# Performance work log

Hardware: AMD Instinct MI355X
Metric: run time of the kernel (lower is better)

Reference implementation:

```python
import jax, jax.numpy as jnp
import numpy as np

B, S, D, A, O = 4, 4096, 256, 64, 256

def setup_inputs() -> dict:
    key = jax.random.key(0)
    k1, k2, k3, k4, k5 = jax.random.split(key, 5)
    x = jax.random.normal(k1, (B, S, D), dtype=jnp.float32)
    # weights stored as [in, out] so projection is x @ W (same math as torch Linear W^T)
    Wk = jax.random.normal(k2, (D, A), dtype=jnp.float32) * (1.0 / np.sqrt(D))
    Wq = jax.random.normal(k3, (D, A), dtype=jnp.float32) * (1.0 / np.sqrt(D))
    Wv = jax.random.normal(k4, (D, A), dtype=jnp.float32) * (1.0 / np.sqrt(D))
    Wo = jax.random.normal(k5, (A, O), dtype=jnp.float32) * (1.0 / np.sqrt(A))
    return {"x": x, "Wk": Wk, "Wq": Wq, "Wv": Wv, "Wo": Wo}

def reference(x, Wk, Wq, Wv, Wo):
    # Single-head self-attention; dropout is identity at inference.
    k = x @ Wk  # [B,S,A]
    q = x @ Wq  # [B,S,A]
    v = x @ Wv  # [B,S,A]
    scale = 1.0 / jnp.sqrt(jnp.asarray(A, x.dtype))
    # logits[b,s,t] = k[b,s,:] . q[b,t,:]   (K @ Q^T in the torch code)
    logits = jnp.einsum('bsa,bta->bst', k, q) * scale
    w = jax.nn.softmax(logits, axis=-1)  # softmax over t
    # out[b,s,:] = sum_t w[b,s,t] * v[b,t,:]  (equivalent to V @ w^T then transpose)
    attn = jnp.einsum('bst,bta->bsa', w, v)
    return attn @ Wo  # [B,S,O]
```

## Files before the change

### kernel.cpp

```cpp
#include <hip/hip_runtime.h>


#define SQN 4096
#define AN 64

typedef short bf16x8 __attribute__((ext_vector_type(8)));
typedef float f32x4 __attribute__((ext_vector_type(4)));

__device__ __forceinline__ unsigned short f2bf(float f) {
    unsigned int u = __float_as_uint(f);
    u += 0x7fffu + ((u >> 16) & 1u);
    return (unsigned short)(u >> 16);
}
__device__ __forceinline__ unsigned int cvtpk(float lo, float hi) {
    unsigned int r;
    asm("v_cvt_pk_bf16_f32 %0, %1, %2" : "=v"(r) : "v"(lo), "v"(hi));
    return r;
}
__device__ __forceinline__ float exp2_hw(float x) {
    float r; asm("v_exp_f32 %0, %1" : "=v"(r) : "v"(x)); return r;
}

__global__ __launch_bounds__(256) void k_wtrans(
    const float* __restrict__ Wk, const float* __restrict__ Wq,
    const float* __restrict__ Wv, const float* __restrict__ Wo,
    unsigned short* __restrict__ WT, unsigned short* __restrict__ WoT)
{
    int bidx = blockIdx.x, tid = threadIdx.x;
    if (bidx < 24) {
        int m = bidx >> 3, chunk = bidx & 7;
        const float* src = (m == 0) ? Wk : (m == 1) ? Wq : Wv;
        float scl = (m == 1) ? 0.18033688011112042f : 1.0f;
        unsigned short* dst = WT + (m * 64 + chunk * 8) * 256;
        for (int idx = tid; idx < 8 * 256; idx += 256) {
            int a = chunk * 8 + (idx >> 8), d = idx & 255;
            dst[idx] = f2bf(src[d * 64 + a] * scl);
        }
    } else {
        int chunk = bidx - 24;
        for (int idx = tid; idx < 32 * 64; idx += 256) {
            int o = chunk * 32 + (idx >> 6), a = idx & 63;
            WoT[o * 64 + a] = f2bf(Wo[a * 256 + o]);
        }
    }
}

__global__ __launch_bounds__(256) void k_proj(
    const float* __restrict__ x, const unsigned short* __restrict__ WT,
    unsigned short* __restrict__ Ko, unsigned short* __restrict__ Qo,
    unsigned short* __restrict__ VTo)
{
    __shared__ unsigned short x_lds[32 * 256];
    const int tid = threadIdx.x;
    const int wid = tid >> 6, lane = tid & 63, g = lane >> 4, li = lane & 15;
    const int s0 = blockIdx.x * 32;

    {
        const float4* xs = (const float4*)(x + (size_t)s0 * 256);
        #pragma unroll
        for (int i = 0; i < 8; ++i) {
            int idx4 = i * 256 + tid;
            float4 v = xs[idx4];
            int row = idx4 >> 6, q = idx4 & 63;
            int unit = q >> 1, half = q & 1;
            uint2 u; u.x = cvtpk(v.x, v.y); u.y = cvtpk(v.z, v.w);
            *(uint2*)&x_lds[row * 256 + ((unit ^ (row & 7)) << 3) + half * 4] = u;
        }
    }
    __syncthreads();

    f32x4 acc[3][2] = {};
    #pragma unroll
    for (int dc = 0; dc < 8; ++dc) {
        bf16x8 afr[2];
        #pragma unroll
        for (int sf = 0; sf < 2; ++sf) {
            int ar = sf * 16 + li;
            afr[sf] = *(const bf16x8*)&x_lds[ar * 256 + (((4 * dc + g) ^ (ar & 7)) << 3)];
        }
        #pragma unroll
        for (int c = 0; c < 3; ++c) {
            int wc = (wid * 3 + c) * 16 + li;
            bf16x8 bfr = *(const bf16x8*)&WT[wc * 256 + dc * 32 + 8 * g];
            #pragma unroll
            for (int sf = 0; sf < 2; ++sf)
                acc[c][sf] = __builtin_amdgcn_mfma_f32_16x16x32_bf16(afr[sf], bfr, acc[c][sf], 0, 0, 0);
        }
    }

    const int b = s0 >> 12;
    #pragma unroll
    for (int c = 0; c < 3; ++c) {
        int cfg = wid * 3 + c;
        int p = cfg >> 2, col = (cfg & 3) * 16 + li;
        if (p == 2) {
            #pragma unroll
            for (int sf = 0; sf < 2; ++sf) {
                int sb = (s0 & 4095) + sf * 16 + 4 * g;
                uint2 u;
                u.x = cvtpk(acc[c][sf][0], acc[c][sf][1]);
                u.y = cvtpk(acc[c][sf][2], acc[c][sf][3]);
                *(uint2*)&VTo[(((size_t)(b * 64 + col)) << 12) + sb] = u;
            }
        } else {
            unsigned short* dst = (p == 0) ? Ko : Qo;
            #pragma unroll
            for (int sf = 0; sf < 2; ++sf)
                #pragma unroll
                for (int r = 0; r < 4; ++r)
                    dst[(size_t)(s0 + sf * 16 + 4 * g + r) * 64 + col] = f2bf(acc[c][sf][r]);
        }
    }
}

__global__ __launch_bounds__(1024, 4) void k_attn(
    const unsigned short* __restrict__ Qg, const unsigned short* __restrict__ Kg,
    const unsigned short* __restrict__ VTg, const unsigned short* __restrict__ WoT,
    float* __restrict__ out)
{
    __shared__ unsigned short q_lds[4][4][2048];
    __shared__ unsigned short v_lds[4][4][2048];
    __shared__ unsigned int   p_lds[16][256];

    const int tid = threadIdx.x;
    const int wid = tid >> 6, lane = tid & 63, g = lane >> 4, li = lane & 15;
    const int grp = wid >> 2, ws = wid & 3;
    const int b = blockIdx.x >> 6;
    const int s0 = (blockIdx.x & 63) * 64;
    const int t_beg = grp * 1024;
    const size_t base = (size_t)b * SQN * AN;

    const int gtid = tid & 255;
    const int qrow = gtid >> 3, qseg = gtid & 7;
    const int vrow = gtid >> 2, vseg = gtid & 3;
    const int q_woff = qrow * 64 + ((qseg ^ (qrow & 7)) << 3);
    const int v_woff = vrow * 32 + (((vseg + ((vrow >> 1) & 3)) & 3) << 3);
    const unsigned short* qg0 = Qg + base + (size_t)(t_beg + qrow) * 64 + qseg * 8;
    const unsigned short* vg0 = VTg + (((size_t)(b * 64 + vrow)) << 12) + t_beg + vseg * 8;

    bf16x8 kfrag[2];
    {
        const unsigned short* kp = Kg + base + (size_t)(s0 + ws * 16 + li) * 64;
        kfrag[0] = *(const bf16x8*)(kp + 8 * g);
        kfrag[1] = *(const bf16x8*)(kp + 32 + 8 * g);
    }

    f32x4 ot[4] = {};
    float m_run = -1e30f, l_run = 0.0f;

    {
        uint4 q0 = *(const uint4*)(qg0);
        uint4 v0 = *(const uint4*)(vg0);
        *(uint4*)&q_lds[grp][0][q_woff] = q0;
        *(uint4*)&v_lds[grp][0][v_woff] = v0;
    }
    uint4 qsA = *(const uint4*)(qg0 + 2048);
    uint4 vsA = *(const uint4*)(vg0 + 32);
    uint4 qsB = {}, vsB = {};

    auto compute = [&](int i) {
        const unsigned short* qb = &q_lds[grp][i & 3][0];
        const unsigned short* vb = &v_lds[grp][i & 3][0];
        f32x4 st[2];
        #pragma unroll
        for (int tf = 0; tf < 2; ++tf) {
            int row = tf * 16 + li;
            bf16x8 qa0 = *(const bf16x8*)&qb[row * 64 + ((g ^ (row & 7)) << 3)];
            bf16x8 qa1 = *(const bf16x8*)&qb[row * 64 + (((4 + g) ^ (row & 7)) << 3)];
            f32x4 a0 = {};
            a0 = __builtin_amdgcn_mfma_f32_16x16x32_bf16(qa0, kfrag[0], a0, 0, 0, 0);
            a0 = __builtin_amdgcn_mfma_f32_16x16x32_bf16(qa1, kfrag[1], a0, 0, 0, 0);
            st[tf] = a0;
        }
        float tm = fmaxf(fmaxf(fmaxf(st[0][0], st[0][1]), fmaxf(st[0][2], st[0][3])),
                         fmaxf(fmaxf(st[1][0], st[1][1]), fmaxf(st[1][2], st[1][3])));
        tm = fmaxf(tm, __shfl_xor(tm, 16));
        tm = fmaxf(tm, __shfl_xor(tm, 32));
        if (__any(tm > m_run + 8.0f)) {
            float m_new = fmaxf(m_run, tm);
            float alpha = exp2_hw(m_run - m_new);
            #pragma unroll
            for (int af = 0; af < 4; ++af) {
                ot[af][0] *= alpha; ot[af][1] *= alpha;
                ot[af][2] *= alpha; ot[af][3] *= alpha;
            }
            l_run *= alpha;
            m_run = m_new;
        }
        float ts = 0.0f;
        #pragma unroll
        for (int tf = 0; tf < 2; ++tf) {
            float p0 = exp2_hw(st[tf][0] - m_run);
            float p1 = exp2_hw(st[tf][1] - m_run);
            float p2 = exp2_hw(st[tf][2] - m_run);
            float p3 = exp2_hw(st[tf][3] - m_run);
            ts += (p0 + p1) + (p2 + p3);
            uint2 u; u.x = cvtpk(p0, p1); u.y = cvtpk(p2, p3);
            int w0 = 8 * tf + 2 * g;
            int su = ((w0 >> 2) + ((li >> 1) & 3)) & 3;
            *(uint2*)&p_lds[wid][li * 16 + (su << 2) + (w0 & 3)] = u;
        }
        ts += __shfl_xor(ts, 16);
        ts += __shfl_xor(ts, 32);
        l_run += ts;
        union { uint4 u4; bf16x8 v; } pb;
        pb.u4 = *(const uint4*)&p_lds[wid][li * 16 + (((g + ((li >> 1) & 3)) & 3) << 2)];
        #pragma unroll
        for (int af = 0; af < 4; ++af) {
            int row = af * 16 + li;
            bf16x8 va = *(const bf16x8*)&vb[row * 32 + (((g + ((row >> 1) & 3)) & 3) << 3)];
            ot[af] = __builtin_amdgcn_mfma_f32_16x16x32_bf16(va, pb.v, ot[af], 0, 0, 0);
        }
    };

    for (int i = 0; i < 32; i += 2) {
        {
            *(uint4*)&q_lds[grp][(i + 1) & 3][q_woff] = qsA;
            *(uint4*)&v_lds[grp][(i + 1) & 3][v_woff] = vsA;
            if (i < 30) {
                qsB = *(const uint4*)(qg0 + (size_t)(i + 2) * 2048);
                vsB = *(const uint4*)(vg0 + (i + 2) * 32);
            }
            __syncthreads();
            compute(i);
        }
        {
            if (i + 1 < 31) {
                *(uint4*)&q_lds[grp][(i + 2) & 3][q_woff] = qsB;
                *(uint4*)&v_lds[grp][(i + 2) & 3][v_woff] = vsB;
            }
            if (i + 1 < 30) {
                qsA = *(const uint4*)(qg0 + (size_t)(i + 3) * 2048);
                vsA = *(const uint4*)(vg0 + (i + 3) * 32);
            }
            __syncthreads();
            compute(i + 1);
        }
    }

    __syncthreads();
    float* o_part = (float*)&q_lds[0][0][0];
    float* ml = (float*)&p_lds[0][0];
    unsigned short* a_lds = (unsigned short*)(ml + 512);

    {
        int s_loc = ws * 16 + li;
        float* op = o_part + (size_t)(grp * 64 + s_loc) * 64;
        #pragma unroll
        for (int af = 0; af < 4; ++af) {
            int lu = 4 * af + g;
            float4 o;
            o.x = ot[af][0]; o.y = ot[af][1]; o.z = ot[af][2]; o.w = ot[af][3];
            *(float4*)(op + ((lu ^ (s_loc & 7)) << 2)) = o;
        }
        if (g == 0) {
            ml[grp * 64 + s_loc] = m_run;
            ml[256 + grp * 64 + s_loc] = l_run;
        }
    }
    __syncthreads();

    {
        int row = tid >> 4, ac = (tid & 15) * 4;
        float mm[4], ll[4];
        #pragma unroll
        for (int h = 0; h < 4; ++h) {
            mm[h] = ml[h * 64 + row];
            ll[h] = ml[256 + h * 64 + row];
        }
        float M = fmaxf(fmaxf(mm[0], mm[1]), fmaxf(mm[2], mm[3]));
        float w[4], denom = 0.0f;
        #pragma unroll
        for (int h = 0; h < 4; ++h) { w[h] = exp2_hw(mm[h] - M); denom += w[h] * ll[h]; }
        float inv = 1.0f / denom;
        float4 av = {0.f, 0.f, 0.f, 0.f};
        #pragma unroll
        for (int h = 0; h < 4; ++h) {
            float4 v = *(const float4*)&o_part[(size_t)(h * 64 + row) * 64 + (((ac >> 2) ^ (row & 7)) << 2)];
            av.x += w[h] * v.x; av.y += w[h] * v.y; av.z += w[h] * v.z; av.w += w[h] * v.w;
        }
        int unit = ac >> 3;
        uint2 u; u.x = cvtpk(av.x * inv, av.y * inv); u.y = cvtpk(av.z * inv, av.w * inv);
        *(uint2*)&a_lds[row * 64 + ((unit ^ (row & 7)) << 3) + (ac & 7)] = u;
    }
    __syncthreads();

    {
        int row = grp * 16 + li;
        bf16x8 b0 = *(const bf16x8*)&a_lds[row * 64 + ((g ^ (row & 7)) << 3)];
        bf16x8 b1 = *(const bf16x8*)&a_lds[row * 64 + (((4 + g) ^ (row & 7)) << 3)];
        #pragma unroll
        for (int of = 0; of < 4; ++of) {
            const unsigned short* wp = WoT + (size_t)(ws * 64 + of * 16 + li) * 64;
            bf16x8 w0 = *(const bf16x8*)(wp + 8 * g);
            bf16x8 w1 = *(const bf16x8*)(wp + 32 + 8 * g);
            f32x4 acc = {};
            acc = __builtin_amdgcn_mfma_f32_16x16x32_bf16(w0, b0, acc, 0, 0, 0);
            acc = __builtin_amdgcn_mfma_f32_16x16x32_bf16(w1, b1, acc, 0, 0, 0);
            float4 o;
            o.x = acc[0]; o.y = acc[1]; o.z = acc[2]; o.w = acc[3];
            *(float4*)&out[((size_t)b * 4096 + s0 + grp * 16 + li) * 256 + ws * 64 + of * 16 + 4 * g] = o;
        }
    }
}

extern "C" void kernel_launch(void* const* d_in, const int* in_sizes, int n_in,
                              void* d_out, int out_size, void* d_ws, size_t ws_size,
                              hipStream_t stream) {
    const float* x  = (const float*)d_in[0];
    const float* Wk = (const float*)d_in[1];
    const float* Wq = (const float*)d_in[2];
    const float* Wv = (const float*)d_in[3];
    const float* Wo = (const float*)d_in[4];
    float* out = (float*)d_out;

    char* ws = (char*)d_ws;
    unsigned short* WT  = (unsigned short*)(ws);
    unsigned short* WoT = (unsigned short*)(ws + 98304);
    unsigned short* Qb  = (unsigned short*)(ws + 131072);
    unsigned short* Kb  = (unsigned short*)(ws + 131072 + (1u<<21));
    unsigned short* VTb = (unsigned short*)(ws + 131072 + (2u<<21));

    k_wtrans<<<32, 256, 0, stream>>>(Wk, Wq, Wv, Wo, WT, WoT);
    k_proj<<<512, 256, 0, stream>>>(x, WT, Kb, Qb, VTb);
    k_attn<<<256, 1024, 0, stream>>>(Qb, Kb, VTb, WoT, out);
}
```

Before: 122.4 us.

## Restructure attention kernel: 8 key-split groups, 32 query rows per wave, register P

```diff
diff --git a/kernel.cpp b/kernel.cpp
--- a/kernel.cpp
+++ b/kernel.cpp
@@ -118,164 +118,191 @@
     const unsigned short* __restrict__ VTg, const unsigned short* __restrict__ WoT,
     float* __restrict__ out)
 {
-    __shared__ unsigned short q_lds[4][4][2048];
-    __shared__ unsigned short v_lds[4][4][2048];
-    __shared__ unsigned int   p_lds[16][256];
+    __shared__ __attribute__((aligned(16))) char smem[143360];
+    unsigned short* q_lds = (unsigned short*)smem;
+    unsigned short* v_lds = (unsigned short*)(smem + 65536);
+    float* ml            = (float*)(smem + 131072);
+    unsigned short* a_lds = (unsigned short*)(smem + 135168);
+    float* o_part        = (float*)smem;
 
     const int tid = threadIdx.x;
     const int wid = tid >> 6, lane = tid & 63, g = lane >> 4, li = lane & 15;
-    const int grp = wid >> 2, ws = wid & 3;
-    const int b = blockIdx.x >> 6;
-    const int s0 = (blockIdx.x & 63) * 64;
-    const int t_beg = grp * 1024;
+    const int grp = wid >> 1, ws = wid & 1;
+    const int xcd = blockIdx.x & 7, idx = blockIdx.x >> 3;
+    const int b = xcd >> 1;
+    const int s0 = ((xcd & 1) * 32 + idx) * 64;
+    const int t_beg = grp * 512;
     const size_t base = (size_t)b * SQN * AN;
 
-    const int gtid = tid & 255;
-    const int qrow = gtid >> 3, qseg = gtid & 7;
-    const int vrow = gtid >> 2, vseg = gtid & 3;
-    const int q_woff = qrow * 64 + ((qseg ^ (qrow & 7)) << 3);
-    const int v_woff = vrow * 32 + (((vseg + ((vrow >> 1) & 3)) & 3) << 3);
-    const unsigned short* qg0 = Qg + base + (size_t)(t_beg + qrow) * 64 + qseg * 8;
-    const unsigned short* vg0 = VTg + (((size_t)(b * 64 + vrow)) << 12) + t_beg + vseg * 8;
-
-    bf16x8 kfrag[2];
-    {
-        const unsigned short* kp = Kg + base + (size_t)(s0 + ws * 16 + li) * 64;
-        kfrag[0] = *(const bf16x8*)(kp + 8 * g);
-        kfrag[1] = *(const bf16x8*)(kp + 32 + 8 * g);
-    }
-
-    f32x4 ot[4] = {};
-    float m_run = -1e30f, l_run = 0.0f;
-
-    {
-        uint4 q0 = *(const uint4*)(qg0);
-        uint4 v0 = *(const uint4*)(vg0);
-        *(uint4*)&q_lds[grp][0][q_woff] = q0;
-        *(uint4*)&v_lds[grp][0][v_woff] = v0;
-    }
-    uint4 qsA = *(const uint4*)(qg0 + 2048);
-    uint4 vsA = *(const uint4*)(vg0 + 32);
-    uint4 qsB = {}, vsB = {};
-
-    auto compute = [&](int i) {
-        const unsigned short* qb = &q_lds[grp][i & 3][0];
-        const unsigned short* vb = &v_lds[grp][i & 3][0];
-        f32x4 st[2];
+    const int gt = tid & 127;
+    const int qrow = gt >> 2, qseg = gt & 3;
+    const int vrow = gt >> 1, vhalf = gt & 1;
+    const int qo0 = qrow * 64 + (((2 * qseg)     ^ (qrow & 7)) << 3);
+    const int qo1 = qrow * 64 + (((2 * qseg + 1) ^ (qrow & 7)) << 3);
+    const int vrot = (vrow >> 1) & 3;
+    const int u0 = 2 * vhalf, u1 = 2 * vhalf + 1;
+    const int vo00 = vrow * 32 + (((2 * u0     + vrot) & 3) << 3) + ((u0 >> 1) << 2);
+    const int vo01 = vrow * 32 + (((2 * u0 + 1 + vrot) & 3) << 3) + ((u0 >> 1) << 2);
+    const int vo10 = vrow * 32 + (((2 * u1     + vrot) & 3) << 3) + ((u1 >> 1) << 2);
+    const int vo11 = vrow * 32 + (((2 * u1 + 1 + vrot) & 3) << 3) + ((u1 >> 1) << 2);
+    const unsigned short* qg0 = Qg + base + (size_t)(t_beg + qrow) * 64 + qseg * 16;
+    const unsigned short* vg0 = VTg + (((size_t)(b * 64 + vrow)) << 12) + t_beg + vhalf * 16;
+
+    bf16x8 kf[2][2];
+    #pragma unroll
+    for (int sf = 0; sf < 2; ++sf) {
+        const unsigned short* kp = Kg + base + (size_t)(s0 + ws * 32 + sf * 16 + li) * 64;
+        kf[sf][0] = *(const bf16x8*)(kp + 8 * g);
+        kf[sf][1] = *(const bf16x8*)(kp + 32 + 8 * g);
+    }
+
+    uint4 q0, q1, v0, v1;
+    auto issue = [&](int t4) {
+        const unsigned short* qp = qg0 + (size_t)t4 * 2048;
+        const unsigned short* vp = vg0 + t4 * 32;
+        q0 = *(const uint4*)(qp); q1 = *(const uint4*)(qp + 8);
+        v0 = *(const uint4*)(vp); v1 = *(const uint4*)(vp + 8);
+    };
+    auto stage_write = [&](int buf) {
+        unsigned short* qb = q_lds + (grp * 2 + buf) * 2048;
+        unsigned short* vb = v_lds + (grp * 2 + buf) * 2048;
+        *(uint4*)&qb[qo0] = q0;
+        *(uint4*)&qb[qo1] = q1;
+        uint2 a, b2;
+        a.x = v0.x; a.y = v0.y; b2.x = v0.z; b2.y = v0.w;
+        *(uint2*)&vb[vo00] = a; *(uint2*)&vb[vo01] = b2;
+        a.x = v1.x; a.y = v1.y; b2.x = v1.z; b2.y = v1.w;
+        *(uint2*)&vb[vo10] = a; *(uint2*)&vb[vo11] = b2;
+    };
+
+    f32x4 ot[4][2] = {};
+    float m_run[2] = {-1e30f, -1e30f}, l_run[2] = {0.0f, 0.0f};
+
+    issue(0);
+    stage_write(0);
+    issue(1);
+    __syncthreads();
+
+    for (int i = 0; i < 16; ++i) {
+        if (i < 15) stage_write((i + 1) & 1);
+
+        const unsigned short* qb = q_lds + (grp * 2 + (i & 1)) * 2048;
+        const unsigned short* vb = v_lds + (grp * 2 + (i & 1)) * 2048;
+
+        bf16x8 qa[2][2];
         #pragma unroll
         for (int tf = 0; tf < 2; ++tf) {
             int row = tf * 16 + li;
-            bf16x8 qa0 = *(const bf16x8*)&qb[row * 64 + ((g ^ (row & 7)) << 3)];
-            bf16x8 qa1 = *(const bf16x8*)&qb[row * 64 + (((4 + g) ^ (row & 7)) << 3)];
-            f32x4 a0 = {};
-            a0 = __builtin_amdgcn_mfma_f32_16x16x32_bf16(qa0, kfrag[0], a0, 0, 0, 0);
-            a0 = __builtin_amdgcn_mfma_f32_16x16x32_bf16(qa1, kfrag[1], a0, 0, 0, 0);
-            st[tf] = a0;
-        }
-        float tm = fmaxf(fmaxf(fmaxf(st[0][0], st[0][1]), fmaxf(st[0][2], st[0][3])),
-                         fmaxf(fmaxf(st[1][0], st[1][1]), fmaxf(st[1][2], st[1][3])));
-        tm = fmaxf(tm, __shfl_xor(tm, 16));
-        tm = fmaxf(tm, __shfl_xor(tm, 32));
-        if (__any(tm > m_run + 8.0f)) {
-            float m_new = fmaxf(m_run, tm);
-            float alpha = exp2_hw(m_run - m_new);
-            #pragma unroll
-            for (int af = 0; af < 4; ++af) {
-                ot[af][0] *= alpha; ot[af][1] *= alpha;
-                ot[af][2] *= alpha; ot[af][3] *= alpha;
-            }
-            l_run *= alpha;
-            m_run = m_new;
-        }
-        float ts = 0.0f;
-        #pragma unroll
-        for (int tf = 0; tf < 2; ++tf) {
-            float p0 = exp2_hw(st[tf][0] - m_run);
-            float p1 = exp2_hw(st[tf][1] - m_run);
-            float p2 = exp2_hw(st[tf][2] - m_run);
-            float p3 = exp2_hw(st[tf][3] - m_run);
-            ts += (p0 + p1) + (p2 + p3);
-            uint2 u; u.x = cvtpk(p0, p1); u.y = cvtpk(p2, p3);
-            int w0 = 8 * tf + 2 * g;
-            int su = ((w0 >> 2) + ((li >> 1) & 3)) & 3;
-            *(uint2*)&p_lds[wid][li * 16 + (su << 2) + (w0 & 3)] = u;
-        }
-        ts += __shfl_xor(ts, 16);
-        ts += __shfl_xor(ts, 32);
-        l_run += ts;
-        union { uint4 u4; bf16x8 v; } pb;
-        pb.u4 = *(const uint4*)&p_lds[wid][li * 16 + (((g + ((li >> 1) & 3)) & 3) << 2)];
+            qa[tf][0] = *(const bf16x8*)&qb[row * 64 + ((g ^ (row & 7)) << 3)];
+            qa[tf][1] = *(const bf16x8*)&qb[row * 64 + (((4 + g) ^ (row & 7)) << 3)];
+        }
+        if (i < 14) issue(i + 2);
+
+        f32x4 st[2][2] = {};
+        #pragma unroll
+        for (int tf = 0; tf < 2; ++tf)
+            #pragma unroll
+            for (int sf = 0; sf < 2; ++sf) {
+                st[tf][sf] = __builtin_amdgcn_mfma_f32_16x16x32_bf16(qa[tf][0], kf[sf][0], st[tf][sf], 0, 0, 0);
+                st[tf][sf] = __builtin_amdgcn_mfma_f32_16x16x32_bf16(qa[tf][1], kf[sf][1], st[tf][sf], 0, 0, 0);
+            }
+
+        float tm[2];
+        #pragma unroll
+        for (int sf = 0; sf < 2; ++sf) {
+            float a = fmaxf(fmaxf(st[0][sf][0], st[0][sf][1]), fmaxf(st[0][sf][2], st[0][sf][3]));
+            float c = fmaxf(fmaxf(st[1][sf][0], st[1][sf][1]), fmaxf(st[1][sf][2], st[1][sf][3]));
+            float t = fmaxf(a, c);
+            t = fmaxf(t, __shfl_xor(t, 16));
+            t = fmaxf(t, __shfl_xor(t, 32));
+            tm[sf] = t;
+        }
+        bool need = (tm[0] > m_run[0] + 8.0f) || (tm[1] > m_run[1] + 8.0f);
+        if (__any(need)) {
+            #pragma unroll
+            for (int sf = 0; sf < 2; ++sf) {
+                float m_new = fmaxf(m_run[sf], tm[sf]);
+                float alpha = exp2_hw(m_run[sf] - m_new);
+                #pragma unroll
+                for (int af = 0; af < 4; ++af) {
+                    ot[af][sf][0] *= alpha; ot[af][sf][1] *= alpha;
+                    ot[af][sf][2] *= alpha; ot[af][sf][3] *= alpha;
+                }
+                l_run[sf] *= alpha;
+                m_run[sf] = m_new;
+            }
+        }
+
+        union { unsigned int w[4]; bf16x8 v; } pb[2];
+        #pragma unroll
+        for (int sf = 0; sf < 2; ++sf) {
+            float p0 = exp2_hw(st[0][sf][0] - m_run[sf]);
+            float p1 = exp2_hw(st[0][sf][1] - m_run[sf]);
+            float p2 = exp2_hw(st[0][sf][2] - m_run[sf]);
+            float p3 = exp2_hw(st[0][sf][3] - m_run[sf]);
+            float p4 = exp2_hw(st[1][sf][0] - m_run[sf]);
+            float p5 = exp2_hw(st[1][sf][1] - m_run[sf]);
+            float p6 = exp2_hw(st[1][sf][2] - m_run[sf]);
+            float p7 = exp2_hw(st[1][sf][3] - m_run[sf]);
+            float ts = ((p0 + p1) + (p2 + p3)) + ((p4 + p5) + (p6 + p7));
+            pb[sf].w[0] = cvtpk(p0, p1); pb[sf].w[1] = cvtpk(p2, p3);
+            pb[sf].w[2] = cvtpk(p4, p5); pb[sf].w[3] = cvtpk(p6, p7);
+            ts += __shfl_xor(ts, 16);
+            ts += __shfl_xor(ts, 32);
+            l_run[sf] += ts;
+        }
+
         #pragma unroll
         for (int af = 0; af < 4; ++af) {
             int row = af * 16 + li;
             bf16x8 va = *(const bf16x8*)&vb[row * 32 + (((g + ((row >> 1) & 3)) & 3) << 3)];
-            ot[af] = __builtin_amdgcn_mfma_f32_16x16x32_bf16(va, pb.v, ot[af], 0, 0, 0);
-        }
-    };
-
-    for (int i = 0; i < 32; i += 2) {
-        {
-            *(uint4*)&q_lds[grp][(i + 1) & 3][q_woff] = qsA;
-            *(uint4*)&v_lds[grp][(i + 1) & 3][v_woff] = vsA;
-            if (i < 30) {
-                qsB = *(const uint4*)(qg0 + (size_t)(i + 2) * 2048);
-                vsB = *(const uint4*)(vg0 + (i + 2) * 32);
-            }
-            __syncthreads();
-            compute(i);
-        }
-        {
-            if (i + 1 < 31) {
-                *(uint4*)&q_lds[grp][(i + 2) & 3][q_woff] = qsB;
-                *(uint4*)&v_lds[grp][(i + 2) & 3][v_woff] = vsB;
-            }
-            if (i + 1 < 30) {
-                qsA = *(const uint4*)(qg0 + (size_t)(i + 3) * 2048);
-                vsA = *(const uint4*)(vg0 + (i + 3) * 32);
-            }
-            __syncthreads();
-            compute(i + 1);
-        }
-    }
-
-    __syncthreads();
-    float* o_part = (float*)&q_lds[0][0][0];
-    float* ml = (float*)&p_lds[0][0];
-    unsigned short* a_lds = (unsigned short*)(ml + 512);
+            #pragma unroll
+            for (int sf = 0; sf < 2; ++sf)
+                ot[af][sf] = __builtin_amdgcn_mfma_f32_16x16x32_bf16(va, pb[sf].v, ot[af][sf], 0, 0, 0);
+        }
+
+        __syncthreads();
+    }
 
     {
-        int s_loc = ws * 16 + li;
-        float* op = o_part + (size_t)(grp * 64 + s_loc) * 64;
-        #pragma unroll
-        for (int af = 0; af < 4; ++af) {
-            int lu = 4 * af + g;
-            float4 o;
-            o.x = ot[af][0]; o.y = ot[af][1]; o.z = ot[af][2]; o.w = ot[af][3];
-            *(float4*)(op + ((lu ^ (s_loc & 7)) << 2)) = o;
-        }
-        if (g == 0) {
-            ml[grp * 64 + s_loc] = m_run;
-            ml[256 + grp * 64 + s_loc] = l_run;
+        #pragma unroll
+        for (int sf = 0; sf < 2; ++sf) {
+            int s_loc = ws * 32 + sf * 16 + li;
+            float* op = o_part + (size_t)(grp * 64 + s_loc) * 64;
+            #pragma unroll
+            for (int af = 0; af < 4; ++af) {
+                int lu = 4 * af + g;
+                float4 o;
+                o.x = ot[af][sf][0]; o.y = ot[af][sf][1];
+                o.z = ot[af][sf][2]; o.w = ot[af][sf][3];
+                *(float4*)(op + ((lu ^ (s_loc & 7)) << 2)) = o;
+            }
+            if (g == 0) {
+                ml[grp * 64 + s_loc] = m_run[sf];
+                ml[512 + grp * 64 + s_loc] = l_run[sf];
+            }
         }
     }
     __syncthreads();
 
     {
         int row = tid >> 4, ac = (tid & 15) * 4;
-        float mm[4], ll[4];
-        #pragma unroll
-        for (int h = 0; h < 4; ++h) {
+        float mm[8], ll[8];
+        #pragma unroll
+        for (int h = 0; h < 8; ++h) {
             mm[h] = ml[h * 64 + row];
-            ll[h] = ml[256 + h * 64 + row];
-        }
-        float M = fmaxf(fmaxf(mm[0], mm[1]), fmaxf(mm[2], mm[3]));
-        float w[4], denom = 0.0f;
-        #pragma unroll
-        for (int h = 0; h < 4; ++h) { w[h] = exp2_hw(mm[h] - M); denom += w[h] * ll[h]; }
+            ll[h] = ml[512 + h * 64 + row];
+        }
+        float M = mm[0];
+        #pragma unroll
+        for (int h = 1; h < 8; ++h) M = fmaxf(M, mm[h]);
+        float w[8], denom = 0.0f;
+        #pragma unroll
+        for (int h = 0; h < 8; ++h) { w[h] = exp2_hw(mm[h] - M); denom += w[h] * ll[h]; }
         float inv = 1.0f / denom;
         float4 av = {0.f, 0.f, 0.f, 0.f};
         #pragma unroll
-        for (int h = 0; h < 4; ++h) {
+        for (int h = 0; h < 8; ++h) {
             float4 v = *(const float4*)&o_part[(size_t)(h * 64 + row) * 64 + (((ac >> 2) ^ (row & 7)) << 2)];
             av.x += w[h] * v.x; av.y += w[h] * v.y; av.z += w[h] * v.z; av.w += w[h] * v.w;
         }
@@ -286,12 +313,13 @@
     __syncthreads();
 
     {
-        int row = grp * 16 + li;
+        int sq = wid >> 2, oq = wid & 3;
+        int row = sq * 16 + li;
         bf16x8 b0 = *(const bf16x8*)&a_lds[row * 64 + ((g ^ (row & 7)) << 3)];
         bf16x8 b1 = *(const bf16x8*)&a_lds[row * 64 + (((4 + g) ^ (row & 7)) << 3)];
         #pragma unroll
         for (int of = 0; of < 4; ++of) {
-            const unsigned short* wp = WoT + (size_t)(ws * 64 + of * 16 + li) * 64;
+            const unsigned short* wp = WoT + (size_t)(oq * 64 + of * 16 + li) * 64;
             bf16x8 w0 = *(const bf16x8*)(wp + 8 * g);
             bf16x8 w1 = *(const bf16x8*)(wp + 32 + 8 * g);
             f32x4 acc = {};
@@ -299,7 +327,7 @@
             acc = __builtin_amdgcn_mfma_f32_16x16x32_bf16(w1, b1, acc, 0, 0, 0);
             float4 o;
             o.x = acc[0]; o.y = acc[1]; o.z = acc[2]; o.w = acc[3];
-            *(float4*)&out[((size_t)b * 4096 + s0 + grp * 16 + li) * 256 + ws * 64 + of * 16 + 4 * g] = o;
+            *(float4*)&out[((size_t)b * 4096 + s0 + sq * 16 + li) * 256 + oq * 64 + of * 16 + 4 * g] = o;
         }
     }
 }
```

Measured after the change: 122.5 us. No clear change (+0.1%).
